# Optimization experiments

Measured on AMD Instinct MI355X. Metric: run time of the kernel, lower is better.

## Reference

```python
import jax, jax.numpy as jnp
import numpy as np

B, N, PREV, PRED, H = 16, 64, 6, 30, 256
E = N * (N - 1)
BN_EPS = 1e-5


def _mlp(x, W1, b1, W2, b2, gamma, beta):
    # Two-layer ELU MLP with batch norm over flattened (batch*rows) dim.
    h = jax.nn.elu(x @ W1 + b1)
    h = jax.nn.elu(h @ W2 + b2)
    b, n, d = h.shape
    f = h.reshape(b * n, d)
    mu = f.mean(axis=0)
    var = f.var(axis=0)
    f = (f - mu) * jax.lax.rsqrt(var + BN_EPS) * gamma + beta
    return f.reshape(b, n, d)


def setup_inputs() -> dict:
    key = jax.random.key(0)
    ks = jax.random.split(key, 8)
    # fully-connected directed graph without self loops
    recv, send = np.where(~np.eye(N, dtype=bool))  # each [E]
    rel_rec = jnp.broadcast_to(jax.nn.one_hot(jnp.asarray(recv), N)[None], (B, E, N)).astype(jnp.float32)
    rel_send = jnp.broadcast_to(jax.nn.one_hot(jnp.asarray(send), N)[None], (B, E, N)).astype(jnp.float32)

    def xavier(k, shape):
        fan_in, fan_out = shape
        std = np.sqrt(2.0 / (fan_in + fan_out))
        return jax.random.normal(k, shape, jnp.float32) * std

    return {
        "prev_actor_centers": jax.random.normal(ks[0], (B, N, PREV, 2), jnp.float32) * 10.0,
        "rel_rec": rel_rec,
        "rel_send": rel_send,
        "W_traj": xavier(ks[1], (PREV * 2, H)),
        "b_traj": jnp.full((H,), 0.1, jnp.float32),
        "n2e_W1": xavier(ks[2], (2 * H, H)),
        "n2e_b1": jnp.full((H,), 0.1, jnp.float32),
        "n2e_W2": xavier(ks[3], (H, H)),
        "n2e_b2": jnp.full((H,), 0.1, jnp.float32),
        "n2e_gamma": jnp.ones((H,), jnp.float32),
        "n2e_beta": jnp.zeros((H,), jnp.float32),
        "e2n_W1": xavier(ks[4], (2 * H, H)),
        "e2n_b1": jnp.full((H,), 0.1, jnp.float32),
        "e2n_W2": xavier(ks[5], (H, H)),
        "e2n_b2": jnp.full((H,), 0.1, jnp.float32),
        "e2n_gamma": jnp.ones((H,), jnp.float32),
        "e2n_beta": jnp.zeros((H,), jnp.float32),
        "W_fuse": xavier(ks[6], (2 * H, H)),
        "b_fuse": jnp.full((H,), 0.1, jnp.float32),
        "W_pred": xavier(ks[7], (H, PRED * 2)),
        "b_pred": jnp.full((PRED * 2,), 0.1, jnp.float32),
    }


def reference(prev_actor_centers, rel_rec, rel_send,
              W_traj, b_traj,
              n2e_W1, n2e_b1, n2e_W2, n2e_b2, n2e_gamma, n2e_beta,
              e2n_W1, e2n_b1, e2n_W2, e2n_b2, e2n_gamma, e2n_beta,
              W_fuse, b_fuse, W_pred, b_pred):
    b, n, prev, _ = prev_actor_centers.shape
    # relative displacements, first step zero
    diffs = prev_actor_centers[:, :, 1:, :] - prev_actor_centers[:, :, :-1, :]
    rel_pos = jnp.concatenate([jnp.zeros((b, n, 1, 2), prev_actor_centers.dtype), diffs], axis=2)
    rel_pos = rel_pos.reshape(b, n, prev * 2)
    x = rel_pos @ W_traj + b_traj  # [b, n, H] node features

    # node2edge: gather via one-hot relation matmuls
    receivers = jnp.einsum('ben,bnh->beh', rel_rec, x)
    senders = jnp.einsum('ben,bnh->beh', rel_send, x)
    edges = jnp.concatenate([receivers, senders], axis=-1)  # [b, E, 2H]
    e = _mlp(edges, n2e_W1, n2e_b1, n2e_W2, n2e_b2, n2e_gamma, n2e_beta)

    # edge2node: degree-normalized scatter via transposed relation matmuls
    deg_rec = rel_rec.sum(axis=1)  # [b, n]
    deg_rec = deg_rec + (deg_rec == 0).astype(deg_rec.dtype)
    incoming = jnp.einsum('ben,beh->bnh', rel_rec, e) / deg_rec[..., None]
    deg_send = rel_send.sum(axis=1)
    deg_send = deg_send + (deg_send == 0).astype(deg_send.dtype)
    outgoing = jnp.einsum('ben,beh->bnh', rel_send, e) / deg_send[..., None]
    nodes = jnp.concatenate([incoming, outgoing], axis=-1)  # [b, n, 2H]
    m = _mlp(nodes, e2n_W1, e2n_b1, e2n_W2, e2n_b2, e2n_gamma, e2n_beta)

    fused = jnp.concatenate([x, m], axis=-1) @ W_fuse + b_fuse  # [b, n, H]
    rel = fused @ W_pred + b_pred  # [b, n, PRED*2]

    current_loc = prev_actor_centers[:, :, -1, :]  # [b, n, 2]
    current_loc = jnp.broadcast_to(current_loc[:, :, None, :], (b, n, PRED, 2)).reshape(b, n, PRED * 2)
    pos = jnp.cumsum(rel.reshape(b, n, PRED, 2), axis=2).reshape(b, n, PRED * 2) + current_loc
    return (rel, pos)
```

## Files before the change

### kernel.cpp

```cpp
#include <hip/hip_runtime.h>
#include <hip/hip_bf16.h>

#define BB 16
#define NN 64
#define PREVN 6
#define PREDN 30
#define HH 256
#define EE 4032
#define EROWS (BB*EE)
#define NROWS (BB*NN)

typedef short short8 __attribute__((ext_vector_type(8)));
typedef float f32x4 __attribute__((ext_vector_type(4)));

enum : int {
  OFF_STATS_E = 0,
  OFF_STATS_M = 1024,
  OFF_XRS     = 2048,
  F32_END     = 264192
};
enum : size_t {
  BO_W1TE  = 0,
  BO_W2TE  = 131072,
  BO_W1TN  = 196608,
  BO_W2TN  = 327680,
  BO_WFT   = 393216,
  BO_WPT   = 524288,
  BO_XG    = 540672,
  BO_NODES = 802816,
  BO_H1G   = 1327104,
  BO_M2    = 1589248,
  BO_FG    = 1851392,
  BO_E2    = 2113536
};

__device__ __forceinline__ float eluf(float v) { return v > 0.f ? v : __expf(v) - 1.f; }

__device__ __forceinline__ void gl2lds16(const void* g, void* l) {
  __builtin_amdgcn_global_load_lds(
      (const __attribute__((address_space(1))) void*)g,
      (__attribute__((address_space(3))) void*)l, 16, 0, 0);
}

__device__ __forceinline__ float xembed(const float* __restrict__ centers,
                                        const float* __restrict__ Wt,
                                        const float* __restrict__ bt,
                                        int rr, int col) {
  const float* c = centers + rr * 12;
  float acc = bt[col];
  #pragma unroll
  for (int t = 0; t < 5; ++t) {
    float dx = c[(t+1)*2 + 0] - c[t*2 + 0];
    float dy = c[(t+1)*2 + 1] - c[t*2 + 1];
    acc += dx * Wt[(2 + 2*t)*HH + col] + dy * Wt[(3 + 2*t)*HH + col];
  }
  return acc;
}

struct PrepArgs {
  const float *n2e_W1, *n2e_W2, *e2n_W1, *e2n_W2, *W_fuse, *W_pred;
  float* ws;
  __hip_bfloat16 *w1te, *w2te, *w1tn, *w2tn, *wft, *wpt;
};

__global__ __launch_bounds__(256) void k_prep(PrepArgs a) {
  __shared__ float t[64][65];
  const int bid = blockIdx.x, tid = threadIdx.x;
  if (bid < 128) {
    const float* W; __hip_bfloat16* WT; int K, lb;
    if (bid < 32)      { W = a.n2e_W1; WT = a.w1te; K = 512; lb = bid; }
    else if (bid < 48) { W = a.n2e_W2; WT = a.w2te; K = 256; lb = bid - 32; }
    else if (bid < 80) { W = a.e2n_W1; WT = a.w1tn; K = 512; lb = bid - 48; }
    else if (bid < 96) { W = a.e2n_W2; WT = a.w2tn; K = 256; lb = bid - 80; }
    else               { W = a.W_fuse; WT = a.wft;  K = 512; lb = bid - 96; }
    int KB = K / 64;
    int k0 = (lb % KB) * 64, n0 = (lb / KB) * 64;
    int tx = tid & 63, ty = tid >> 6;
    #pragma unroll
    for (int i = 0; i < 16; ++i)
      t[ty + i*4][tx] = W[(size_t)(k0 + ty + i*4) * 256 + n0 + tx];
    __syncthreads();
    #pragma unroll
    for (int i = 0; i < 16; ++i)
      WT[(size_t)(n0 + ty + i*4) * K + k0 + tx] = __float2bfloat16(t[tx][ty + i*4]);
  } else if (bid < 192) {
    int idx = (bid - 128) * 256 + tid;
    int c = idx >> 8, k = idx & 255;
    a.wpt[idx] = __float2bfloat16(c < 60 ? a.W_pred[k * 60 + c] : 0.f);
  } else {
    a.ws[(bid - 192) * 256 + tid] = 0.f;
  }
}

__global__ __launch_bounds__(256) void k_xrs(
    const float* __restrict__ centers,
    const float* __restrict__ W_traj,
    const float* __restrict__ b_traj,
    const __hip_bfloat16* __restrict__ W1T,
    const float* __restrict__ b1,
    __hip_bfloat16* __restrict__ xrs,
    __hip_bfloat16* __restrict__ xg) {
  __shared__ alignas(16) __hip_bfloat16 xls[32][264];
  const int tid = threadIdx.x;
  const int w = tid >> 6, lane = tid & 63;
  const int m16 = lane & 15, quad = lane >> 4;
  const int ko = quad * 8;
  const int half = blockIdx.x >> 5;
  const int row0 = (blockIdx.x & 31) * 32;
  const int colw = w * 64;
  __hip_bfloat16* dst = xrs + (size_t)half * 262144;

  #pragma unroll 4
  for (int r = 0; r < 32; ++r)
    xls[r][tid] = __float2bfloat16(xembed(centers, W_traj, b_traj, row0 + r, tid));
  __syncthreads();

  if (half == 0) {
    #pragma unroll
    for (int i = 0; i < 4; ++i) {
      int u = i*256 + tid;
      int r = u >> 5, c = (u & 31) * 8;
      *reinterpret_cast<uint4*>(xg + (size_t)(row0 + r)*256 + c) =
          *reinterpret_cast<const uint4*>(&xls[r][c]);
    }
  }

  f32x4 acc[2][4];
  #pragma unroll
  for (int jt = 0; jt < 4; ++jt) {
    float bv = half ? 0.f : b1[colw + jt*16 + m16];
    #pragma unroll
    for (int mt = 0; mt < 2; ++mt) acc[mt][jt] = (f32x4){bv, bv, bv, bv};
  }
  #pragma unroll
  for (int ks = 0; ks < 8; ++ks) {
    short8 af[2], bf[4];
    #pragma unroll
    for (int mt = 0; mt < 2; ++mt)
      af[mt] = *reinterpret_cast<const short8*>(&xls[mt*16 + m16][ks*32 + ko]);
    #pragma unroll
    for (int jt = 0; jt < 4; ++jt)
      bf[jt] = *reinterpret_cast<const short8*>(
          W1T + (size_t)(colw + jt*16 + m16)*512 + half*256 + ks*32 + ko);
    #pragma unroll
    for (int mt = 0; mt < 2; ++mt)
      #pragma unroll
      for (int jt = 0; jt < 4; ++jt)
        acc[mt][jt] = __builtin_amdgcn_mfma_f32_16x16x32_bf16(af[mt], bf[jt],
                                                              acc[mt][jt], 0, 0, 0);
  }
  #pragma unroll
  for (int mt = 0; mt < 2; ++mt)
    #pragma unroll
    for (int jt = 0; jt < 4; ++jt)
      #pragma unroll
      for (int r = 0; r < 4; ++r)
        dst[(size_t)(row0 + mt*16 + quad*4 + r)*256 + colw + jt*16 + m16] =
            __float2bfloat16(acc[mt][jt][r]);
}

__global__ __launch_bounds__(256, 2) void k_mlp6(
    const __hip_bfloat16* __restrict__ xrs,
    const __hip_bfloat16* __restrict__ W2T,
    const float* __restrict__ b2,
    __hip_bfloat16* __restrict__ outp,
    float* __restrict__ stats) {
  __shared__ alignas(16) char reg1[33792];
  __shared__ alignas(16) __hip_bfloat16 h1s[64][264];
  __shared__ float sst[2][256];
  const int tid = threadIdx.x;
  const int w = tid >> 6, lane = tid & 63;
  const int m16 = lane & 15, quad = lane >> 4;
  const int ko = quad * 8;
  const int blk = blockIdx.x;
  const int bb = blk / 63, lb = blk - bb*63;
  const int row0 = blk * 64;
  const int n0 = (lb * 64) / 63;
  const int colw = w * 64;

  const char* xsb = (const char*)(xrs + 262144 + (size_t)bb*64*256);
  #pragma unroll
  for (int i = 0; i < 8; ++i) {
    int seg = w*8 + i;
    gl2lds16(xsb + seg*1024 + lane*16, reg1 + seg*1024);
  }
  if (w == 0)
    gl2lds16((const char*)(xrs + (size_t)(bb*64 + n0)*256) + lane*16, reg1 + 32768);
  sst[0][tid] = 0.f;
  sst[1][tid] = 0.f;
  __syncthreads();

  {
    const int ty = tid >> 7;
    const int c2 = (tid & 127) * 2;
    #pragma unroll 4
    for (int r2 = 0; r2 < 32; ++r2) {
      int r = ty*32 + r2;
      int e = lb*64 + r;
      int rc = e / 63; int jj = e - rc*63;
      int sd = jj + (jj >= rc ? 1 : 0);
      __hip_bfloat162 xa = *reinterpret_cast<const __hip_bfloat162*>(
          reg1 + 32768 + (rc - n0)*512 + c2*2);
      __hip_bfloat162 xs2 = *reinterpret_cast<const __hip_bfloat162*>(
          reg1 + sd*512 + c2*2);
      __hip_bfloat162 o;
      o.x = __float2bfloat16(eluf(__bfloat162float(xa.x) + __bfloat162float(xs2.x)));
      o.y = __float2bfloat16(eluf(__bfloat162float(xa.y) + __bfloat162float(xs2.y)));
      *reinterpret_cast<__hip_bfloat162*>(&h1s[r][c2]) = o;
    }
  }
  __syncthreads();

  f32x4 acc2[4][4];
  #pragma unroll
  for (int jt = 0; jt < 4; ++jt) {
    float bv = b2[colw + jt*16 + m16];
    #pragma unroll
    for (int mt = 0; mt < 4; ++mt) acc2[mt][jt] = (f32x4){bv, bv, bv, bv};
  }
  #pragma unroll
  for (int kt = 0; kt < 4; ++kt) {
    #pragma unroll
    for (int ks = 0; ks < 2; ++ks) {
      const int k0 = kt*64 + ks*32 + ko;
      short8 af[4], bf[4];
      #pragma unroll
      for (int jt = 0; jt < 4; ++jt)
        bf[jt] = *reinterpret_cast<const short8*>(
            W2T + (size_t)(colw + jt*16 + m16)*256 + k0);
      #pragma unroll
      for (int mt = 0; mt < 4; ++mt)
        af[mt] = *(const short8*)((const char*)h1s +
                     (size_t)(mt*16 + m16)*528 + k0*2);
      #pragma unroll
      for (int mt = 0; mt < 4; ++mt)
        #pragma unroll
        for (int jt = 0; jt < 4; ++jt)
          acc2[mt][jt] = __builtin_amdgcn_mfma_f32_16x16x32_bf16(af[mt], bf[jt],
                                                                 acc2[mt][jt], 0, 0, 0);
    }
  }
  __syncthreads();

  #pragma unroll
  for (int jt = 0; jt < 4; ++jt) {
    float ps = 0.f, pq = 0.f;
    #pragma unroll
    for (int mt = 0; mt < 4; ++mt)
      #pragma unroll
      for (int r = 0; r < 4; ++r) {
        float hv = eluf(acc2[mt][jt][r]);
        h1s[mt*16 + quad*4 + r][colw + jt*16 + m16] = __float2bfloat16(hv);
        ps += hv; pq += hv * hv;
      }
    atomicAdd(&sst[0][colw + jt*16 + m16], ps);
    atomicAdd(&sst[1][colw + jt*16 + m16], pq);
  }
  __syncthreads();

  atomicAdd(&stats[tid], sst[0][tid]);
  atomicAdd(&stats[256 + tid], sst[1][tid]);
  #pragma unroll
  for (int i = 0; i < 8; ++i) {
    int u = i*256 + tid;
    int r = u >> 5, c = (u & 31) * 8;
    *reinterpret_cast<uint4*>(outp + (size_t)(row0 + r)*HH + c) =
        *reinterpret_cast<const uint4*>(&h1s[r][c]);
  }
}

__global__ __launch_bounds__(1024) void k_agg2(const __hip_bfloat16* __restrict__ e2,
                                               const float* __restrict__ st,
                                               const float* __restrict__ gam,
                                               const float* __restrict__ bet,
                                               __hip_bfloat16* __restrict__ nodes) {
  __shared__ float red[32][256];
  const int blk = blockIdx.x;
  const int bn = blk >> 1, half = blk & 1;
  const int b = bn >> 6, n = bn & 63;
  const int tid = threadIdx.x;
  const int c8 = (tid & 31) * 8;
  const int rg = tid >> 5;
  const __hip_bfloat16* base = e2 + (size_t)b * EE * HH;
  float s[8] = {0.f,0.f,0.f,0.f,0.f,0.f,0.f,0.f};
  for (int j = rg; j < 63; j += 32) {
    const __hip_bfloat16* rp;
    if (half == 0) {
      rp = base + (size_t)(n*63 + j)*HH;
    } else {
      int i = j + (j >= n ? 1 : 0);
      int e = i*63 + n - (n > i ? 1 : 0);
      rp = base + (size_t)e*HH;
    }
    union { uint4 u; __hip_bfloat16 h[8]; } v;
    v.u = *reinterpret_cast<const uint4*>(rp + c8);
    #pragma unroll
    for (int jj = 0; jj < 8; ++jj) s[jj] += __bfloat162float(v.h[jj]);
  }
  #pragma unroll
  for (int jj = 0; jj < 8; jj += 4)
    *reinterpret_cast<float4*>(&red[rg][c8 + jj]) =
        (float4){s[jj], s[jj+1], s[jj+2], s[jj+3]};
  __syncthreads();
  if (tid < 256) {
    float S = 0.f;
    #pragma unroll
    for (int r = 0; r < 32; ++r) S += red[r][tid];
    const float inv = 1.f / (float)EROWS;
    float mean = st[tid] * inv;
    float var  = fmaxf(st[256 + tid] * inv - mean*mean, 0.f);
    float a = gam[tid] * rsqrtf(var + 1e-5f);
    float c0 = bet[tid] - mean * a;
    nodes[(size_t)bn*512 + half*256 + tid] = __float2bfloat16(a * S * (1.f/63.f) + c0);
  }
}

__global__ __launch_bounds__(64) void k_n1(
    const __hip_bfloat16* __restrict__ nodes,
    const __hip_bfloat16* __restrict__ W1T,
    const float* __restrict__ b1,
    __hip_bfloat16* __restrict__ h1g) {
  __shared__ alignas(16) __hip_bfloat16 hls[16][72];
  const int lane = threadIdx.x;
  const int m16 = lane & 15, quad = lane >> 4;
  const int ko = quad * 8;
  const int row0 = (blockIdx.x >> 2) * 16;
  const int j0 = (blockIdx.x & 3) * 64;

  f32x4 acc[4];
  #pragma unroll
  for (int jt = 0; jt < 4; ++jt) {
    float bv = b1[j0 + jt*16 + m16];
    acc[jt] = (f32x4){bv, bv, bv, bv};
  }
  #pragma unroll
  for (int ks = 0; ks < 16; ++ks) {
    short8 af = *reinterpret_cast<const short8*>(
        nodes + (size_t)(row0 + m16)*512 + ks*32 + ko);
    short8 bf[4];
    #pragma unroll
    for (int jt = 0; jt < 4; ++jt)
      bf[jt] = *reinterpret_cast<const short8*>(
          W1T + (size_t)(j0 + jt*16 + m16)*512 + ks*32 + ko);
    #pragma unroll
    for (int jt = 0; jt < 4; ++jt)
      acc[jt] = __builtin_amdgcn_mfma_f32_16x16x32_bf16(af, bf[jt], acc[jt], 0, 0, 0);
  }
  #pragma unroll
  for (int jt = 0; jt < 4; ++jt)
    #pragma unroll
    for (int r = 0; r < 4; ++r)
      hls[quad*4 + r][jt*16 + m16] = __float2bfloat16(eluf(acc[jt][r]));
  #pragma unroll
  for (int i = 0; i < 2; ++i) {
    int u = i*64 + lane;
    int r = u >> 3, c = (u & 7) * 8;
    *reinterpret_cast<uint4*>(h1g + (size_t)(row0 + r)*256 + j0 + c) =
        *reinterpret_cast<const uint4*>(&hls[r][c]);
  }
}

__global__ __launch_bounds__(64) void k_n2(
    const __hip_bfloat16* __restrict__ h1g,
    const __hip_bfloat16* __restrict__ W2T,
    const float* __restrict__ b2,
    __hip_bfloat16* __restrict__ m2,
    float* __restrict__ stats) {
  __shared__ alignas(16) __hip_bfloat16 hls[16][72];
  __shared__ float sst[2][64];
  const int lane = threadIdx.x;
  const int m16 = lane & 15, quad = lane >> 4;
  const int ko = quad * 8;
  const int row0 = (blockIdx.x >> 2) * 16;
  const int j0 = (blockIdx.x & 3) * 64;

  sst[0][lane] = 0.f;
  sst[1][lane] = 0.f;

  f32x4 acc[4];
  #pragma unroll
  for (int jt = 0; jt < 4; ++jt) {
    float bv = b2[j0 + jt*16 + m16];
    acc[jt] = (f32x4){bv, bv, bv, bv};
  }
  #pragma unroll
  for (int ks = 0; ks < 8; ++ks) {
    short8 af = *reinterpret_cast<const short8*>(
        h1g + (size_t)(row0 + m16)*256 + ks*32 + ko);
    short8 bf[4];
    #pragma unroll
    for (int jt = 0; jt < 4; ++jt)
      bf[jt] = *reinterpret_cast<const short8*>(
          W2T + (size_t)(j0 + jt*16 + m16)*256 + ks*32 + ko);
    #pragma unroll
    for (int jt = 0; jt < 4; ++jt)
      acc[jt] = __builtin_amdgcn_mfma_f32_16x16x32_bf16(af, bf[jt], acc[jt], 0, 0, 0);
  }
  #pragma unroll
  for (int jt = 0; jt < 4; ++jt) {
    float ps = 0.f, pq = 0.f;
    #pragma unroll
    for (int r = 0; r < 4; ++r) {
      float hv = eluf(acc[jt][r]);
      hls[quad*4 + r][jt*16 + m16] = __float2bfloat16(hv);
      ps += hv; pq += hv * hv;
    }
    atomicAdd(&sst[0][jt*16 + m16], ps);
    atomicAdd(&sst[1][jt*16 + m16], pq);
  }
  atomicAdd(&stats[j0 + lane], sst[0][lane]);
  atomicAdd(&stats[256 + j0 + lane], sst[1][lane]);
  #pragma unroll
  for (int i = 0; i < 2; ++i) {
    int u = i*64 + lane;
    int r = u >> 3, c = (u & 7) * 8;
    *reinterpret_cast<uint4*>(m2 + (size_t)(row0 + r)*256 + j0 + c) =
        *reinterpret_cast<const uint4*>(&hls[r][c]);
  }
}

__global__ __launch_bounds__(64) void k_hf(
    const __hip_bfloat16* __restrict__ xg,
    const __hip_bfloat16* __restrict__ m2,
    const float* __restrict__ stM,
    const float* __restrict__ gam,
    const float* __restrict__ bet,
    const __hip_bfloat16* __restrict__ WfT,
    const float* __restrict__ bfv,
    __hip_bfloat16* __restrict__ fg) {
  __shared__ alignas(16) __hip_bfloat16 hls[16][72];
  __shared__ float bnA[256], bnC[256];
  const int lane = threadIdx.x;
  const int m16 = lane & 15, quad = lane >> 4;
  const int ko = quad * 8;
  const int row0 = (blockIdx.x >> 2) * 16;
  const int j0 = (blockIdx.x & 3) * 64;

  {
    const float inv = 1.f / (float)NROWS;
    #pragma unroll
    for (int j = 0; j < 4; ++j) {
      int k = lane*4 + j;
      float mean = stM[k] * inv;
      float var  = fmaxf(stM[256 + k] * inv - mean*mean, 0.f);
      float am = gam[k] * rsqrtf(var + 1e-5f);
      bnA[k] = am;
      bnC[k] = bet[k] - mean * am;
    }
  }

  f32x4 acc[4];
  #pragma unroll
  for (int jt = 0; jt < 4; ++jt) {
    float bv = bfv[j0 + jt*16 + m16];
    acc[jt] = (f32x4){bv, bv, bv, bv};
  }
  #pragma unroll
  for (int ks = 0; ks < 16; ++ks) {
    short8 af;
    if (ks < 8) {
      af = *reinterpret_cast<const short8*>(
          xg + (size_t)(row0 + m16)*256 + ks*32 + ko);
    } else {
      int k0 = (ks - 8)*32 + ko;
      union { uint4 u; __hip_bfloat16 h[8]; } v;
      v.u = *reinterpret_cast<const uint4*>(m2 + (size_t)(row0 + m16)*256 + k0);
      union { short8 s8; __hip_bfloat16 h[8]; } o;
      #pragma unroll
      for (int j = 0; j < 8; ++j)
        o.h[j] = __float2bfloat16(bnA[k0+j] * __bfloat162float(v.h[j]) + bnC[k0+j]);
      af = o.s8;
    }
    short8 bf[4];
    #pragma unroll
    for (int jt = 0; jt < 4; ++jt)
      bf[jt] = *reinterpret_cast<const short8*>(
          WfT + (size_t)(j0 + jt*16 + m16)*512 + ks*32 + ko);
    #pragma unroll
    for (int jt = 0; jt < 4; ++jt)
      acc[jt] = __builtin_amdgcn_mfma_f32_16x16x32_bf16(af, bf[jt], acc[jt], 0, 0, 0);
  }
  #pragma unroll
  for (int jt = 0; jt < 4; ++jt)
    #pragma unroll
    for (int r = 0; r < 4; ++r)
      hls[quad*4 + r][jt*16 + m16] = __float2bfloat16(acc[jt][r]);
  #pragma unroll
  for (int i = 0; i < 2; ++i) {
    int u = i*64 + lane;
    int r = u >> 3, c = (u & 7) * 8;
    *reinterpret_cast<uint4*>(fg + (size_t)(row0 + r)*256 + j0 + c) =
        *reinterpret_cast<const uint4*>(&hls[r][c]);
  }
}

__global__ __launch_bounds__(64) void k_pred(
    const __hip_bfloat16* __restrict__ fg,
    const __hip_bfloat16* __restrict__ WpT,
    const float* __restrict__ bp,
    const float* __restrict__ centers,
    float* __restrict__ out) {
  __shared__ float rl[16][68];
  const int lane = threadIdx.x;
  const int m16 = lane & 15, quad = lane >> 4;
  const int ko = quad * 8;
  const int row0 = blockIdx.x * 16;

  f32x4 acc[4];
  #pragma unroll
  for (int jt = 0; jt < 4; ++jt) {
    int c = jt*16 + m16;
    float bv = (c < 60) ? bp[c] : 0.f;
    acc[jt] = (f32x4){bv, bv, bv, bv};
  }
  #pragma unroll
  for (int ks = 0; ks < 8; ++ks) {
    short8 af = *reinterpret_cast<const short8*>(
        fg + (size_t)(row0 + m16)*256 + ks*32 + ko);
    short8 bf[4];
    #pragma unroll
    for (int jt = 0; jt < 4; ++jt)
      bf[jt] = *reinterpret_cast<const short8*>(
          WpT + (size_t)(jt*16 + m16)*256 + ks*32 + ko);
    #pragma unroll
    for (int jt = 0; jt < 4; ++jt)
      acc[jt] = __builtin_amdgcn_mfma_f32_16x16x32_bf16(af, bf[jt], acc[jt], 0, 0, 0);
  }
  #pragma unroll
  for (int jt = 0; jt < 4; ++jt) {
    int c = jt*16 + m16;
    #pragma unroll
    for (int r = 0; r < 4; ++r) {
      int lr = quad*4 + r;
      rl[lr][c] = acc[jt][r];
      if (c < 60) out[(size_t)(row0 + lr)*60 + c] = acc[jt][r];
    }
  }
  if (lane < 32) {
    int lr = lane >> 1, xy = lane & 1;
    int grow = row0 + lr;
    float run = centers[(size_t)(grow*PREVN + 5)*2 + xy];
    #pragma unroll
    for (int p = 0; p < PREDN; ++p) {
      run += rl[lr][2*p + xy];
      out[61440 + (size_t)grow*60 + 2*p + xy] = run;
    }
  }
}

extern "C" void kernel_launch(void* const* d_in, const int* in_sizes, int n_in,
                              void* d_out, int out_size, void* d_ws, size_t ws_size,
                              hipStream_t stream) {
  const float* centers = (const float*)d_in[0];
  float* ws = (float*)d_ws;
  __hip_bfloat16* wb = (__hip_bfloat16*)(ws + F32_END);
  __hip_bfloat16* xrs = (__hip_bfloat16*)(ws + OFF_XRS);

  const float* W_traj = (const float*)d_in[3];
  const float* b_traj = (const float*)d_in[4];
  const float* n2e_b1 = (const float*)d_in[6];
  const float* n2e_b2 = (const float*)d_in[8];
  const float* n2e_g  = (const float*)d_in[9];
  const float* n2e_be = (const float*)d_in[10];
  const float* e2n_b1 = (const float*)d_in[12];
  const float* e2n_b2 = (const float*)d_in[14];
  const float* e2n_g  = (const float*)d_in[15];
  const float* e2n_be = (const float*)d_in[16];
  const float* b_fuse = (const float*)d_in[18];
  const float* b_pred = (const float*)d_in[20];

  PrepArgs pa;
  pa.n2e_W1 = (const float*)d_in[5];  pa.n2e_W2 = (const float*)d_in[7];
  pa.e2n_W1 = (const float*)d_in[11]; pa.e2n_W2 = (const float*)d_in[13];
  pa.W_fuse = (const float*)d_in[17]; pa.W_pred = (const float*)d_in[19];
  pa.ws = ws;
  pa.w1te = wb + BO_W1TE; pa.w2te = wb + BO_W2TE;
  pa.w1tn = wb + BO_W1TN; pa.w2tn = wb + BO_W2TN;
  pa.wft = wb + BO_WFT;   pa.wpt = wb + BO_WPT;

  k_prep<<<200, 256, 0, stream>>>(pa);
  k_xrs<<<64, 256, 0, stream>>>(centers, W_traj, b_traj, wb + BO_W1TE, n2e_b1,
                                xrs, wb + BO_XG);
  k_mlp6<<<EROWS/64, 256, 0, stream>>>(xrs, wb + BO_W2TE, n2e_b2, wb + BO_E2,
                                       ws + OFF_STATS_E);
  k_agg2<<<2*NROWS, 1024, 0, stream>>>(wb + BO_E2, ws + OFF_STATS_E, n2e_g, n2e_be,
                                       wb + BO_NODES);
  k_n1<<<256, 64, 0, stream>>>(wb + BO_NODES, wb + BO_W1TN, e2n_b1, wb + BO_H1G);
  k_n2<<<256, 64, 0, stream>>>(wb + BO_H1G, wb + BO_W2TN, e2n_b2, wb + BO_M2,
                               ws + OFF_STATS_M);
  k_hf<<<256, 64, 0, stream>>>(wb + BO_XG, wb + BO_M2, ws + OFF_STATS_M,
                               e2n_g, e2n_be, wb + BO_WFT, b_fuse, wb + BO_FG);
  k_pred<<<64, 64, 0, stream>>>(wb + BO_FG, wb + BO_WPT, b_pred, centers,
                                (float*)d_out);
}
```

Measured before the change: 201.7 us.

## Move trajectory embedding into prep, fuse node MLP layers, drop LDS staging in edge kernel

Trajectory embedding now runs in extra k_prep blocks. k_xrs becomes a small one-wave-per-tile MFMA kernel that reads the precomputed embedding. The two node-MLP kernels are merged into k_node, which recomputes the full first-layer hidden tile per column block in LDS, so one launch and one global round trip go away at the cost of four times the first-layer work. k_mlp6 stops staging sender/receiver rows in LDS through global_load_lds, reads them straight from global with precomputed index tables, and raises the occupancy hint to 4 blocks per SM.

```diff
diff --git a/kernel.cpp b/kernel.cpp
--- a/kernel.cpp
+++ b/kernel.cpp
@@ -28,19 +28,12 @@
   BO_WPT   = 524288,
   BO_XG    = 540672,
   BO_NODES = 802816,
-  BO_H1G   = 1327104,
-  BO_M2    = 1589248,
-  BO_FG    = 1851392,
-  BO_E2    = 2113536
+  BO_M2    = 1327104,
+  BO_FG    = 1589248,
+  BO_E2    = 1851392
 };
 
 __device__ __forceinline__ float eluf(float v) { return v > 0.f ? v : __expf(v) - 1.f; }
-
-__device__ __forceinline__ void gl2lds16(const void* g, void* l) {
-  __builtin_amdgcn_global_load_lds(
-      (const __attribute__((address_space(1))) void*)g,
-      (__attribute__((address_space(3))) void*)l, 16, 0, 0);
-}
 
 __device__ __forceinline__ float xembed(const float* __restrict__ centers,
                                         const float* __restrict__ Wt,
@@ -58,9 +51,10 @@
 }
 
 struct PrepArgs {
+  const float *centers, *W_traj, *b_traj;
   const float *n2e_W1, *n2e_W2, *e2n_W1, *e2n_W2, *W_fuse, *W_pred;
   float* ws;
-  __hip_bfloat16 *w1te, *w2te, *w1tn, *w2tn, *wft, *wpt;
+  __hip_bfloat16 *w1te, *w2te, *w1tn, *w2tn, *wft, *wpt, *xg;
 };
 
 __global__ __launch_bounds__(256) void k_prep(PrepArgs a) {
@@ -87,87 +81,67 @@
     int idx = (bid - 128) * 256 + tid;
     int c = idx >> 8, k = idx & 255;
     a.wpt[idx] = __float2bfloat16(c < 60 ? a.W_pred[k * 60 + c] : 0.f);
+  } else if (bid < 200) {
+    a.ws[(bid - 192) * 256 + tid] = 0.f;
   } else {
-    a.ws[(bid - 192) * 256 + tid] = 0.f;
-  }
-}
-
-__global__ __launch_bounds__(256) void k_xrs(
-    const float* __restrict__ centers,
-    const float* __restrict__ W_traj,
-    const float* __restrict__ b_traj,
+    int row0 = (bid - 200) * 16;
+    #pragma unroll
+    for (int r = 0; r < 16; ++r)
+      a.xg[(size_t)(row0 + r)*256 + tid] =
+          __float2bfloat16(xembed(a.centers, a.W_traj, a.b_traj, row0 + r, tid));
+  }
+}
+
+__global__ __launch_bounds__(64) void k_xrs2(
+    const __hip_bfloat16* __restrict__ xg,
     const __hip_bfloat16* __restrict__ W1T,
     const float* __restrict__ b1,
-    __hip_bfloat16* __restrict__ xrs,
-    __hip_bfloat16* __restrict__ xg) {
-  __shared__ alignas(16) __hip_bfloat16 xls[32][264];
-  const int tid = threadIdx.x;
-  const int w = tid >> 6, lane = tid & 63;
+    __hip_bfloat16* __restrict__ xrs) {
+  const int lane = threadIdx.x;
   const int m16 = lane & 15, quad = lane >> 4;
   const int ko = quad * 8;
-  const int half = blockIdx.x >> 5;
-  const int row0 = (blockIdx.x & 31) * 32;
-  const int colw = w * 64;
+  const int rt = blockIdx.x >> 3, s = blockIdx.x & 7;
+  const int half = s >> 2, j0 = (s & 3) * 64;
+  const int row0 = rt * 16;
   __hip_bfloat16* dst = xrs + (size_t)half * 262144;
 
-  #pragma unroll 4
-  for (int r = 0; r < 32; ++r)
-    xls[r][tid] = __float2bfloat16(xembed(centers, W_traj, b_traj, row0 + r, tid));
-  __syncthreads();
-
-  if (half == 0) {
-    #pragma unroll
-    for (int i = 0; i < 4; ++i) {
-      int u = i*256 + tid;
-      int r = u >> 5, c = (u & 31) * 8;
-      *reinterpret_cast<uint4*>(xg + (size_t)(row0 + r)*256 + c) =
-          *reinterpret_cast<const uint4*>(&xls[r][c]);
-    }
-  }
-
-  f32x4 acc[2][4];
-  #pragma unroll
-  for (int jt = 0; jt < 4; ++jt) {
-    float bv = half ? 0.f : b1[colw + jt*16 + m16];
-    #pragma unroll
-    for (int mt = 0; mt < 2; ++mt) acc[mt][jt] = (f32x4){bv, bv, bv, bv};
+  f32x4 acc[4];
+  #pragma unroll
+  for (int jt = 0; jt < 4; ++jt) {
+    float bv = half ? 0.f : b1[j0 + jt*16 + m16];
+    acc[jt] = (f32x4){bv, bv, bv, bv};
   }
   #pragma unroll
   for (int ks = 0; ks < 8; ++ks) {
-    short8 af[2], bf[4];
-    #pragma unroll
-    for (int mt = 0; mt < 2; ++mt)
-      af[mt] = *reinterpret_cast<const short8*>(&xls[mt*16 + m16][ks*32 + ko]);
+    short8 af = *reinterpret_cast<const short8*>(
+        xg + (size_t)(row0 + m16)*256 + ks*32 + ko);
+    short8 bf[4];
     #pragma unroll
     for (int jt = 0; jt < 4; ++jt)
       bf[jt] = *reinterpret_cast<const short8*>(
-          W1T + (size_t)(colw + jt*16 + m16)*512 + half*256 + ks*32 + ko);
-    #pragma unroll
-    for (int mt = 0; mt < 2; ++mt)
-      #pragma unroll
-      for (int jt = 0; jt < 4; ++jt)
-        acc[mt][jt] = __builtin_amdgcn_mfma_f32_16x16x32_bf16(af[mt], bf[jt],
-                                                              acc[mt][jt], 0, 0, 0);
-  }
-  #pragma unroll
-  for (int mt = 0; mt < 2; ++mt)
-    #pragma unroll
-    for (int jt = 0; jt < 4; ++jt)
-      #pragma unroll
-      for (int r = 0; r < 4; ++r)
-        dst[(size_t)(row0 + mt*16 + quad*4 + r)*256 + colw + jt*16 + m16] =
-            __float2bfloat16(acc[mt][jt][r]);
-}
-
-__global__ __launch_bounds__(256, 2) void k_mlp6(
+          W1T + (size_t)(j0 + jt*16 + m16)*512 + half*256 + ks*32 + ko);
+    #pragma unroll
+    for (int jt = 0; jt < 4; ++jt)
+      acc[jt] = __builtin_amdgcn_mfma_f32_16x16x32_bf16(af, bf[jt], acc[jt], 0, 0, 0);
+  }
+  #pragma unroll
+  for (int jt = 0; jt < 4; ++jt)
+    #pragma unroll
+    for (int r = 0; r < 4; ++r)
+      dst[(size_t)(row0 + quad*4 + r)*256 + j0 + jt*16 + m16] =
+          __float2bfloat16(acc[jt][r]);
+}
+
+__global__ __launch_bounds__(256, 4) void k_mlp6(
     const __hip_bfloat16* __restrict__ xrs,
     const __hip_bfloat16* __restrict__ W2T,
     const float* __restrict__ b2,
     __hip_bfloat16* __restrict__ outp,
     float* __restrict__ stats) {
-  __shared__ alignas(16) char reg1[33792];
   __shared__ alignas(16) __hip_bfloat16 h1s[64][264];
   __shared__ float sst[2][256];
+  __shared__ int sd64[64];
+  __shared__ int rcf[64];
   const int tid = threadIdx.x;
   const int w = tid >> 6, lane = tid & 63;
   const int m16 = lane & 15, quad = lane >> 4;
@@ -178,14 +152,12 @@
   const int n0 = (lb * 64) / 63;
   const int colw = w * 64;
 
-  const char* xsb = (const char*)(xrs + 262144 + (size_t)bb*64*256);
-  #pragma unroll
-  for (int i = 0; i < 8; ++i) {
-    int seg = w*8 + i;
-    gl2lds16(xsb + seg*1024 + lane*16, reg1 + seg*1024);
-  }
-  if (w == 0)
-    gl2lds16((const char*)(xrs + (size_t)(bb*64 + n0)*256) + lane*16, reg1 + 32768);
+  if (tid < 64) {
+    int e = lb*64 + tid;
+    int rc = e / 63; int jj = e - rc*63;
+    sd64[tid] = jj + (jj >= rc ? 1 : 0);
+    rcf[tid]  = rc - n0;
+  }
   sst[0][tid] = 0.f;
   sst[1][tid] = 0.f;
   __syncthreads();
@@ -193,16 +165,15 @@
   {
     const int ty = tid >> 7;
     const int c2 = (tid & 127) * 2;
+    const __hip_bfloat16* xrb = xrs + (size_t)(bb*64 + n0)*256 + c2;
+    const __hip_bfloat16* xsb = xrs + 262144 + (size_t)bb*64*256 + c2;
     #pragma unroll 4
     for (int r2 = 0; r2 < 32; ++r2) {
       int r = ty*32 + r2;
-      int e = lb*64 + r;
-      int rc = e / 63; int jj = e - rc*63;
-      int sd = jj + (jj >= rc ? 1 : 0);
       __hip_bfloat162 xa = *reinterpret_cast<const __hip_bfloat162*>(
-          reg1 + 32768 + (rc - n0)*512 + c2*2);
+          xrb + (size_t)rcf[r]*256);
       __hip_bfloat162 xs2 = *reinterpret_cast<const __hip_bfloat162*>(
-          reg1 + sd*512 + c2*2);
+          xsb + (size_t)sd64[r]*256);
       __hip_bfloat162 o;
       o.x = __float2bfloat16(eluf(__bfloat162float(xa.x) + __bfloat162float(xs2.x)));
       o.y = __float2bfloat16(eluf(__bfloat162float(xa.y) + __bfloat162float(xs2.y)));
@@ -315,107 +286,85 @@
   }
 }
 
-__global__ __launch_bounds__(64) void k_n1(
+__global__ __launch_bounds__(64) void k_node(
     const __hip_bfloat16* __restrict__ nodes,
     const __hip_bfloat16* __restrict__ W1T,
     const float* __restrict__ b1,
-    __hip_bfloat16* __restrict__ h1g) {
-  __shared__ alignas(16) __hip_bfloat16 hls[16][72];
-  const int lane = threadIdx.x;
-  const int m16 = lane & 15, quad = lane >> 4;
-  const int ko = quad * 8;
-  const int row0 = (blockIdx.x >> 2) * 16;
-  const int j0 = (blockIdx.x & 3) * 64;
-
-  f32x4 acc[4];
-  #pragma unroll
-  for (int jt = 0; jt < 4; ++jt) {
-    float bv = b1[j0 + jt*16 + m16];
-    acc[jt] = (f32x4){bv, bv, bv, bv};
-  }
-  #pragma unroll
-  for (int ks = 0; ks < 16; ++ks) {
-    short8 af = *reinterpret_cast<const short8*>(
-        nodes + (size_t)(row0 + m16)*512 + ks*32 + ko);
-    short8 bf[4];
-    #pragma unroll
-    for (int jt = 0; jt < 4; ++jt)
-      bf[jt] = *reinterpret_cast<const short8*>(
-          W1T + (size_t)(j0 + jt*16 + m16)*512 + ks*32 + ko);
-    #pragma unroll
-    for (int jt = 0; jt < 4; ++jt)
-      acc[jt] = __builtin_amdgcn_mfma_f32_16x16x32_bf16(af, bf[jt], acc[jt], 0, 0, 0);
-  }
-  #pragma unroll
-  for (int jt = 0; jt < 4; ++jt)
-    #pragma unroll
-    for (int r = 0; r < 4; ++r)
-      hls[quad*4 + r][jt*16 + m16] = __float2bfloat16(eluf(acc[jt][r]));
-  #pragma unroll
-  for (int i = 0; i < 2; ++i) {
-    int u = i*64 + lane;
-    int r = u >> 3, c = (u & 7) * 8;
-    *reinterpret_cast<uint4*>(h1g + (size_t)(row0 + r)*256 + j0 + c) =
-        *reinterpret_cast<const uint4*>(&hls[r][c]);
-  }
-}
-
-__global__ __launch_bounds__(64) void k_n2(
-    const __hip_bfloat16* __restrict__ h1g,
     const __hip_bfloat16* __restrict__ W2T,
     const float* __restrict__ b2,
     __hip_bfloat16* __restrict__ m2,
     float* __restrict__ stats) {
-  __shared__ alignas(16) __hip_bfloat16 hls[16][72];
+  __shared__ alignas(16) __hip_bfloat16 h1[16][264];
+  __shared__ alignas(16) __hip_bfloat16 hl2[16][72];
   __shared__ float sst[2][64];
   const int lane = threadIdx.x;
   const int m16 = lane & 15, quad = lane >> 4;
   const int ko = quad * 8;
-  const int row0 = (blockIdx.x >> 2) * 16;
-  const int j0 = (blockIdx.x & 3) * 64;
+  const int rt = blockIdx.x >> 2;
+  const int j2 = (blockIdx.x & 3) * 64;
+  const int row0 = rt * 16;
 
   sst[0][lane] = 0.f;
   sst[1][lane] = 0.f;
 
-  f32x4 acc[4];
-  #pragma unroll
-  for (int jt = 0; jt < 4; ++jt) {
-    float bv = b2[j0 + jt*16 + m16];
-    acc[jt] = (f32x4){bv, bv, bv, bv};
+  short8 af[16];
+  #pragma unroll
+  for (int ks = 0; ks < 16; ++ks)
+    af[ks] = *reinterpret_cast<const short8*>(
+        nodes + (size_t)(row0 + m16)*512 + ks*32 + ko);
+  #pragma unroll
+  for (int j1 = 0; j1 < 16; ++j1) {
+    float bv = b1[j1*16 + m16];
+    f32x4 acc = (f32x4){bv, bv, bv, bv};
+    #pragma unroll
+    for (int ks = 0; ks < 16; ++ks) {
+      short8 bf = *reinterpret_cast<const short8*>(
+          W1T + (size_t)(j1*16 + m16)*512 + ks*32 + ko);
+      acc = __builtin_amdgcn_mfma_f32_16x16x32_bf16(af[ks], bf, acc, 0, 0, 0);
+    }
+    #pragma unroll
+    for (int r = 0; r < 4; ++r)
+      h1[quad*4 + r][j1*16 + m16] = __float2bfloat16(eluf(acc[r]));
+  }
+
+  f32x4 acc2[4];
+  #pragma unroll
+  for (int jt = 0; jt < 4; ++jt) {
+    float bv = b2[j2 + jt*16 + m16];
+    acc2[jt] = (f32x4){bv, bv, bv, bv};
   }
   #pragma unroll
   for (int ks = 0; ks < 8; ++ks) {
-    short8 af = *reinterpret_cast<const short8*>(
-        h1g + (size_t)(row0 + m16)*256 + ks*32 + ko);
+    short8 a2 = *(const short8*)((const char*)h1 + (size_t)m16*528 + (ks*32 + ko)*2);
     short8 bf[4];
     #pragma unroll
     for (int jt = 0; jt < 4; ++jt)
       bf[jt] = *reinterpret_cast<const short8*>(
-          W2T + (size_t)(j0 + jt*16 + m16)*256 + ks*32 + ko);
-    #pragma unroll
-    for (int jt = 0; jt < 4; ++jt)
-      acc[jt] = __builtin_amdgcn_mfma_f32_16x16x32_bf16(af, bf[jt], acc[jt], 0, 0, 0);
+          W2T + (size_t)(j2 + jt*16 + m16)*256 + ks*32 + ko);
+    #pragma unroll
+    for (int jt = 0; jt < 4; ++jt)
+      acc2[jt] = __builtin_amdgcn_mfma_f32_16x16x32_bf16(a2, bf[jt], acc2[jt], 0, 0, 0);
   }
   #pragma unroll
   for (int jt = 0; jt < 4; ++jt) {
     float ps = 0.f, pq = 0.f;
     #pragma unroll
     for (int r = 0; r < 4; ++r) {
-      float hv = eluf(acc[jt][r]);
-      hls[quad*4 + r][jt*16 + m16] = __float2bfloat16(hv);
+      float hv = eluf(acc2[jt][r]);
+      hl2[quad*4 + r][jt*16 + m16] = __float2bfloat16(hv);
       ps += hv; pq += hv * hv;
     }
     atomicAdd(&sst[0][jt*16 + m16], ps);
     atomicAdd(&sst[1][jt*16 + m16], pq);
   }
-  atomicAdd(&stats[j0 + lane], sst[0][lane]);
-  atomicAdd(&stats[256 + j0 + lane], sst[1][lane]);
+  atomicAdd(&stats[j2 + lane], sst[0][lane]);
+  atomicAdd(&stats[256 + j2 + lane], sst[1][lane]);
   #pragma unroll
   for (int i = 0; i < 2; ++i) {
     int u = i*64 + lane;
     int r = u >> 3, c = (u & 7) * 8;
-    *reinterpret_cast<uint4*>(m2 + (size_t)(row0 + r)*256 + j0 + c) =
-        *reinterpret_cast<const uint4*>(&hls[r][c]);
+    *reinterpret_cast<uint4*>(m2 + (size_t)(row0 + r)*256 + j2 + c) =
+        *reinterpret_cast<const uint4*>(&hl2[r][c]);
   }
 }
 
@@ -570,6 +519,7 @@
   const float* b_pred = (const float*)d_in[20];
 
   PrepArgs pa;
+  pa.centers = centers; pa.W_traj = W_traj; pa.b_traj = b_traj;
   pa.n2e_W1 = (const float*)d_in[5];  pa.n2e_W2 = (const float*)d_in[7];
   pa.e2n_W1 = (const float*)d_in[11]; pa.e2n_W2 = (const float*)d_in[13];
   pa.W_fuse = (const float*)d_in[17]; pa.W_pred = (const float*)d_in[19];
@@ -577,17 +527,17 @@
   pa.w1te = wb + BO_W1TE; pa.w2te = wb + BO_W2TE;
   pa.w1tn = wb + BO_W1TN; pa.w2tn = wb + BO_W2TN;
   pa.wft = wb + BO_WFT;   pa.wpt = wb + BO_WPT;
-
-  k_prep<<<200, 256, 0, stream>>>(pa);
-  k_xrs<<<64, 256, 0, stream>>>(centers, W_traj, b_traj, wb + BO_W1TE, n2e_b1,
-                                xrs, wb + BO_XG);
+  pa.xg = wb + BO_XG;
+
+  k_prep<<<264, 256, 0, stream>>>(pa);
+  k_xrs2<<<512, 64, 0, stream>>>(wb + BO_XG, wb + BO_W1TE, n2e_b1, xrs);
   k_mlp6<<<EROWS/64, 256, 0, stream>>>(xrs, wb + BO_W2TE, n2e_b2, wb + BO_E2,
                                        ws + OFF_STATS_E);
   k_agg2<<<2*NROWS, 1024, 0, stream>>>(wb + BO_E2, ws + OFF_STATS_E, n2e_g, n2e_be,
                                        wb + BO_NODES);
-  k_n1<<<256, 64, 0, stream>>>(wb + BO_NODES, wb + BO_W1TN, e2n_b1, wb + BO_H1G);
-  k_n2<<<256, 64, 0, stream>>>(wb + BO_H1G, wb + BO_W2TN, e2n_b2, wb + BO_M2,
-                               ws + OFF_STATS_M);
+  k_node<<<256, 64, 0, stream>>>(wb + BO_NODES, wb + BO_W1TN, e2n_b1,
+                                 wb + BO_W2TN, e2n_b2, wb + BO_M2,
+                                 ws + OFF_STATS_M);
   k_hf<<<256, 64, 0, stream>>>(wb + BO_XG, wb + BO_M2, ws + OFF_STATS_M,
                                e2n_g, e2n_be, wb + BO_WFT, b_fuse, wb + BO_FG);
   k_pred<<<64, 64, 0, stream>>>(wb + BO_FG, wb + BO_WPT, b_pred, centers,
```

New measurement: 246.9 us. 1.22x slower.
